# Optimization experiments

Measured on AMD Instinct MI355X. Metric: run time of the kernel, lower is better.

The kernel has to match this reference:

```python
import jax, jax.numpy as jnp
import numpy as np
from jax import lax

# ---- static problem constants (match init_kwargs / call_args) ----
T0 = 0.0
T1 = 5_184_000.0            # 60 days in seconds
DT = 60.0                   # Euler step (s)
DT_FORCING = 3600.0         # hourly wind forcing (s)
DTK = 518_400.0             # 6-day reduced-basis window (s)
NSUB = int(DT_FORCING // DT)             # 60 substeps per forcing step
NFORCING = int((T1 - T0) // DT_FORCING)  # 1440 forcing steps
NDT = len(np.arange(T0, T1, DTK))        # 10 basis knots
NL = 1                                   # layers -> K has NL*2 components


def setup_inputs() -> dict:
    key = jax.random.key(0)
    k1, k2, k3 = jax.random.split(key, 3)
    # K = exp(pk); mean -8 keeps exp(pk)*DT << 1 (stable explicit Euler)
    pk = jax.random.normal(k1, (NDT * NL * 2,), jnp.float32) * 0.5 - 8.0
    TAx = jax.random.normal(k2, (NFORCING,), jnp.float32) * 0.1  # wind stress x
    TAy = jax.random.normal(k3, (NFORCING,), jnp.float32) * 0.1  # wind stress y
    fc = jnp.float32(1e-4)  # Coriolis frequency (s^-1)
    return {"pk": pk, "TAx": TAx, "TAy": TAy, "fc": fc}


def _basis_matrix(dtype):
    # pkt2Kt_matrix with base='gauss'
    gptime = jnp.arange(T0 + DTK / 2, T1 + DTK / 2, DTK)   # (NDT,)
    gtime = jnp.arange(T0, T1, DT_FORCING)                 # (NFORCING,)
    distt = gtime[:, None] - gptime[None, :]               # (NFORCING, NDT)
    tmp = jnp.exp(-0.5 * distt ** 2 / DTK ** 2)
    M = tmp / jnp.sum(tmp, axis=1, keepdims=True)
    return M.astype(dtype)


def _forward(pk, TAx, TAy, fc):
    K = jnp.exp(pk).reshape(NDT, NL * 2)          # kt_1D_to_2D
    Kt = _basis_matrix(pk.dtype) @ K               # (NFORCING, NL*2)
    n = TAx.shape[0]

    def vector_field(t, U, V):
        it = (t // DT).astype(jnp.int32)
        itf = it // NSUB
        aa = jnp.mod(it, NSUB) / NSUB
        itsup = jnp.where(itf + 1 >= n, -1, itf + 1)
        tax = (1 - aa) * TAx[itf] + aa * TAx[itsup]
        tay = (1 - aa) * TAy[itf] + aa * TAy[itsup]
        # NB: Kt[it-1] with it up to NFORCING*NSUB relies on jax clamping
        # out-of-range gathers to the last row, exactly as the original.
        Ktnow = (1 - aa) * Kt[it - 1] + aa * Kt[itsup]
        d_U = fc * V + Ktnow[0] * tax - Ktnow[1] * U
        d_V = -fc * U + Ktnow[0] * tay - Ktnow[1] * V
        return d_U, d_V

    def inner(carry, iin):
        U, V, iout = carry
        t = iout * DT_FORCING + iin * DT
        d_U, d_V = vector_field(t, U, V)
        return (U + DT * d_U, V + DT * d_V, iout), None

    def outer(carry, iout):
        U, V = carry
        (u, v, _), _ = lax.scan(inner, (U[iout], V[iout], iout),
                                jnp.arange(NSUB))
        # final update at index NFORCING is out of bounds -> dropped by jax,
        # matching the original module's semantics
        U = U.at[iout + 1].set(u)
        V = V.at[iout + 1].set(v)
        return (U, V), None

    U0 = jnp.zeros(NFORCING, pk.dtype)
    V0 = jnp.zeros(NFORCING, pk.dtype)
    (U, V), _ = lax.scan(outer, (U0, V0), jnp.arange(NFORCING))
    return U, V


def reference(pk, TAx, TAy, fc):
    return _forward(pk, TAx, TAy, fc)
```

## Files before the change

kernel.cpp:

```cpp
#include <hip/hip_runtime.h>
#include <math.h>

#define NF    1440
#define NWIN  1439
#define NSUB  60
#define NDTK  10
#define BLK   256
#define NBLK  6
#define NWAVE (BLK / 64)
#define B0WIN 216
#define TOKEN 0x5AB1A5CAu


__device__ __forceinline__ float2 kt_row(int i, const float* __restrict__ K0,
                                         const float* __restrict__ K1) {
    const float CEXP = -0.5f / 268738560000.0f;
    float gt = 3600.0f * (float)i;
    float s = 0.0f, a0 = 0.0f, a1 = 0.0f;
    #pragma unroll
    for (int j = 0; j < NDTK; ++j) {
        float d = gt - (259200.0f + 518400.0f * (float)j);
        float e = __expf((d * d) * CEXP);
        s += e;
        a0 = fmaf(e, K0[j], a0);
        a1 = fmaf(e, K1[j], a1);
    }
    return make_float2(a0 / s, a1 / s);
}

__device__ __forceinline__ float4 fast_window(float2 ktl, float2 ks,
    float taxa, float dtax, float taya, float dtay, float ci)
{
    const float DT = 60.0f, H = 1.0f / 60.0f;
    const float dk0 = ks.x - ktl.x, dk1 = ks.y - ktl.y;
    const float g0  = DT * ktl.x,  g1  = DT * dk0;
    float cr  = fmaf(-DT, ktl.y, 1.0f);
    const float crinc = (-DT * dk1) * H;
    const float qr1 = fmaf(g0, dtax, g1 * taxa);
    const float qr2 = g1 * dtax;
    const float qi1 = fmaf(g0, dtay, g1 * taya);
    const float qi2 = g1 * dtay;
    float dr  = g0 * taxa;
    float di  = g0 * taya;
    float drD = fmaf(qr2, H * H, qr1 * H);
    float diD = fmaf(qi2, H * H, qi1 * H);
    const float drD2 = 2.0f * qr2 * H * H;
    const float diD2 = 2.0f * qi2 * H * H;
    float Ar = 1.0f, Ai = 0.0f, Br = 0.0f, Bi = 0.0f;
    #pragma unroll 4
    for (int iin = 0; iin < NSUB; ++iin) {
        const float t1 = ci * Ai;
        const float nAr = fmaf(cr, Ar, -t1);
        const float t2 = ci * Ar;
        const float nAi = fmaf(cr, Ai, t2);
        const float t3 = fmaf(-ci, Bi, dr);
        const float nBr = fmaf(cr, Br, t3);
        const float t4 = fmaf(ci, Br, di);
        const float nBi = fmaf(cr, Bi, t4);
        Ar = nAr; Ai = nAi; Br = nBr; Bi = nBi;
        cr += crinc;
        dr += drD; drD += drD2;
        di += diD; diD += diD2;
    }
    return make_float4(Ar, Ai, Br, Bi);
}

__global__ __launch_bounds__(BLK) void slab_lookback_kernel(
    const float* __restrict__ pk,
    const float* __restrict__ TAx,
    const float* __restrict__ TAy,
    const float* __restrict__ fcp,
    float4* __restrict__ agg,
    unsigned int* __restrict__ flags,
    float* __restrict__ out)
{
    const int t    = threadIdx.x;
    const int b    = blockIdx.x;
    const int lane = t & 63;
    const int wid  = t >> 6;
    const float DT = 60.0f;
    const float fc = fcp[0];
    const float ci = -DT * fc;
    const float H  = 1.0f / 60.0f;

    __shared__ float2 sKt[NF];
    __shared__ float4 wagg[NWAVE];
    __shared__ float4 sagg[NBLK];

    float K0[NDTK], K1[NDTK];
    #pragma unroll
    for (int j = 0; j < NDTK; ++j) {
        K0[j] = __expf(pk[2 * j]);
        K1[j] = __expf(pk[2 * j + 1]);
    }

    float Ar = 1.0f, Ai = 0.0f, Br = 0.0f, Bi = 0.0f;
    int ow = -1;

    if (b == 0) {
        for (int i = t; i < NF; i += BLK) sKt[i] = kt_row(i, K0, K1);
        __syncthreads();

        if (t < 64) {
            if (t < 48) {
                const int w = t >> 1;
                const int h = t & 1;
                const float2 ks  = sKt[w + 1];
                const float taxa = TAx[w], dtax = TAx[w + 1] - taxa;
                const float taya = TAy[w], dtay = TAy[w + 1] - taya;
                float fi = (float)(h * 30);
                int   it = w * NSUB + h * 30;
                #pragma unroll 4
                for (int i = 0; i < 30; ++i, ++it) {
                    const int row = (it == 0) ? (NF - 1) : (it - 1);
                    const float2 kta = sKt[row];
                    const float aa  = fi * H;
                    fi += 1.0f;
                    const float tax = fmaf(aa, dtax, taxa);
                    const float tay = fmaf(aa, dtay, taya);
                    const float kt0 = fmaf(aa, ks.x - kta.x, kta.x);
                    const float kt1 = fmaf(aa, ks.y - kta.y, kta.y);
                    const float cr  = fmaf(-DT, kt1, 1.0f);
                    const float g   = DT * kt0;
                    const float dr  = g * tax;
                    const float di  = g * tay;
                    const float t1 = ci * Ai;
                    const float nAr = fmaf(cr, Ar, -t1);
                    const float t2 = ci * Ar;
                    const float nAi = fmaf(cr, Ai, t2);
                    const float t3 = fmaf(-ci, Bi, dr);
                    const float nBr = fmaf(cr, Br, t3);
                    const float t4 = fmaf(ci, Br, di);
                    const float nBi = fmaf(cr, Bi, t4);
                    Ar = nAr; Ai = nAi; Br = nBr; Bi = nBi;
                }
            }
            const float oAr = __shfl_xor(Ar, 1), oAi = __shfl_xor(Ai, 1);
            const float oBr = __shfl_xor(Br, 1), oBi = __shfl_xor(Bi, 1);
            const float cAr = oAr * Ar - oAi * Ai;
            const float cAi = oAr * Ai + oAi * Ar;
            const float cBr = fmaf(oAr, Br, fmaf(-oAi, Bi, oBr));
            const float cBi = fmaf(oAr, Bi, fmaf(oAi, Br, oBi));
            const int src = (2 * t) & 63;
            Ar = __shfl(cAr, src); Ai = __shfl(cAi, src);
            Br = __shfl(cBr, src); Bi = __shfl(cBi, src);
            if (t < 24) {
                ow = t;
            } else {
                Ar = 1.0f; Ai = 0.0f; Br = 0.0f; Bi = 0.0f;
            }
        } else {
            const int w = t - 40;
            const float2 ktl = sKt[NF - 1];
            const float2 ks  = sKt[w + 1];
            const float taxa = TAx[w], dtax = TAx[w + 1] - taxa;
            const float taya = TAy[w], dtay = TAy[w + 1] - taya;
            const float4 W = fast_window(ktl, ks, taxa, dtax, taya, dtay, ci);
            Ar = W.x; Ai = W.y; Br = W.z; Bi = W.w;
            ow = w;
        }
    } else {
        const int w = B0WIN + (b - 1) * BLK + t;
        if (w < NWIN) {
            const float2 ktl = kt_row(NF - 1, K0, K1);
            const float2 ks  = kt_row(w + 1, K0, K1);
            const float taxa = TAx[w], dtax = TAx[w + 1] - taxa;
            const float taya = TAy[w], dtay = TAy[w + 1] - taya;
            const float4 W = fast_window(ktl, ks, taxa, dtax, taya, dtay, ci);
            Ar = W.x; Ai = W.y; Br = W.z; Bi = W.w;
            ow = w;
        }
    }

    float sAr = Ar, sAi = Ai, sBr = Br, sBi = Bi;
    #pragma unroll
    for (int d = 1; d < 64; d <<= 1) {
        const float oAr = __shfl_up(sAr, d);
        const float oAi = __shfl_up(sAi, d);
        const float oBr = __shfl_up(sBr, d);
        const float oBi = __shfl_up(sBi, d);
        if (lane >= d) {
            const float nAr = sAr * oAr - sAi * oAi;
            const float nAi = sAr * oAi + sAi * oAr;
            const float nBr = fmaf(sAr, oBr, fmaf(-sAi, oBi, sBr));
            const float nBi = fmaf(sAr, oBi, fmaf(sAi, oBr, sBi));
            sAr = nAr; sAi = nAi; sBr = nBr; sBi = nBi;
        }
    }
    if (lane == 63) wagg[wid] = make_float4(sAr, sAi, sBr, sBi);
    __syncthreads();

    float eAr = 1.0f, eAi = 0.0f, eBr = 0.0f, eBi = 0.0f;
    for (int q = 0; q < wid; ++q) {
        const float4 g = wagg[q];
        const float nAr = g.x * eAr - g.y * eAi;
        const float nAi = g.x * eAi + g.y * eAr;
        const float nBr = g.x * eBr - g.y * eBi + g.z;
        const float nBi = g.x * eBi + g.y * eBr + g.w;
        eAr = nAr; eAi = nAi; eBr = nBr; eBi = nBi;
    }
    const float tAr = sAr * eAr - sAi * eAi;
    const float tAi = sAr * eAi + sAi * eAr;
    const float tBr = fmaf(sAr, eBr, fmaf(-sAi, eBi, sBr));
    const float tBi = fmaf(sAr, eBi, fmaf(sAi, eBr, sBi));

    if (t == BLK - 1) {
        agg[b] = make_float4(tAr, tAi, tBr, tBi);
        __threadfence();
        __hip_atomic_store(&flags[b], TOKEN, __ATOMIC_RELEASE,
                           __HIP_MEMORY_SCOPE_AGENT);
    }

    if (t < b) {
        while (__hip_atomic_load(&flags[t], __ATOMIC_ACQUIRE,
                                 __HIP_MEMORY_SCOPE_AGENT) != TOKEN) {
            __builtin_amdgcn_s_sleep(1);
        }
        sagg[t] = agg[t];
    }
    __syncthreads();

    float zr = 0.0f, zi = 0.0f;
    for (int j = 0; j < b; ++j) {
        const float4 g = sagg[j];
        const float nzr = fmaf(g.x, zr, fmaf(-g.y, zi, g.z));
        const float nzi = fmaf(g.x, zi, fmaf(g.y, zr, g.w));
        zr = nzr; zi = nzi;
    }

    if (ow >= 0) {
        const float ozr = fmaf(tAr, zr, fmaf(-tAi, zi, tBr));
        const float ozi = fmaf(tAr, zi, fmaf(tAi, zr, tBi));
        out[ow + 1]      = ozr;
        out[NF + ow + 1] = ozi;
    }
    if (b == 0 && t == 0) {
        out[0]  = 0.0f;
        out[NF] = 0.0f;
    }
}

extern "C" void kernel_launch(void* const* d_in, const int* in_sizes, int n_in,
                              void* d_out, int out_size, void* d_ws, size_t ws_size,
                              hipStream_t stream) {
    const float* pk  = (const float*)d_in[0];
    const float* TAx = (const float*)d_in[1];
    const float* TAy = (const float*)d_in[2];
    const float* fcp = (const float*)d_in[3];
    float* out = (float*)d_out;

    float4* agg = (float4*)d_ws;
    unsigned int* flags = (unsigned int*)((char*)d_ws + NBLK * 16);

    slab_lookback_kernel<<<NBLK, BLK, 0, stream>>>(pk, TAx, TAy, fcp,
                                                   agg, flags, out);
}
```

Baseline: 11.30 us.

## Split each window's 60 substeps across two lanes and double block count

Each forcing window's 60-step affine recurrence is now split into two 30-step halves computed by adjacent lanes, combined with a shuffle-xor compose, and the grid grows from 6 to 12 blocks. This halves the serial per-thread chain length, which dominates latency in this small kernel. In exchange, more blocks take part in the decoupled lookback (a longer serial chain of flag waits and aggregate composition), and half the lanes sit idle during the scan. The interpolation start offset for the second half is folded into the initial cr/dr/di terms.

```diff
diff --git a/kernel.cpp b/kernel.cpp
--- a/kernel.cpp
+++ b/kernel.cpp
@@ -6,9 +6,9 @@
 #define NSUB  60
 #define NDTK  10
 #define BLK   256
-#define NBLK  6
+#define NBLK  12
 #define NWAVE (BLK / 64)
-#define B0WIN 216
+#define B0WIN 120
 #define TOKEN 0x5AB1A5CAu
 
 
@@ -28,27 +28,29 @@
     return make_float2(a0 / s, a1 / s);
 }
 
-__device__ __forceinline__ float4 fast_window(float2 ktl, float2 ks,
-    float taxa, float dtax, float taya, float dtay, float ci)
+__device__ __forceinline__ float4 fast_half(float2 ktl, float2 ks,
+    float taxa, float dtax, float taya, float dtay, float ci, float aa0)
 {
     const float DT = 60.0f, H = 1.0f / 60.0f;
     const float dk0 = ks.x - ktl.x, dk1 = ks.y - ktl.y;
     const float g0  = DT * ktl.x,  g1  = DT * dk0;
-    float cr  = fmaf(-DT, ktl.y, 1.0f);
-    const float crinc = (-DT * dk1) * H;
+    const float cr1 = -DT * dk1;
+    float cr  = fmaf(cr1, aa0, fmaf(-DT, ktl.y, 1.0f));
+    const float crinc = cr1 * H;
     const float qr1 = fmaf(g0, dtax, g1 * taxa);
     const float qr2 = g1 * dtax;
     const float qi1 = fmaf(g0, dtay, g1 * taya);
     const float qi2 = g1 * dtay;
-    float dr  = g0 * taxa;
-    float di  = g0 * taya;
-    float drD = fmaf(qr2, H * H, qr1 * H);
-    float diD = fmaf(qi2, H * H, qi1 * H);
+    float dr  = fmaf(fmaf(qr2, aa0, qr1), aa0, g0 * taxa);
+    float di  = fmaf(fmaf(qi2, aa0, qi1), aa0, g0 * taya);
+    const float dstep = (2.0f * aa0 + H) * H;
+    float drD = fmaf(qr2, dstep, qr1 * H);
+    float diD = fmaf(qi2, dstep, qi1 * H);
     const float drD2 = 2.0f * qr2 * H * H;
     const float diD2 = 2.0f * qi2 * H * H;
     float Ar = 1.0f, Ai = 0.0f, Br = 0.0f, Bi = 0.0f;
-    #pragma unroll 4
-    for (int iin = 0; iin < NSUB; ++iin) {
+    #pragma unroll 5
+    for (int iin = 0; iin < 30; ++iin) {
         const float t1 = ci * Ai;
         const float nAr = fmaf(cr, Ar, -t1);
         const float t2 = ci * Ar;
@@ -95,80 +97,82 @@
     }
 
     float Ar = 1.0f, Ai = 0.0f, Br = 0.0f, Bi = 0.0f;
-    int ow = -1;
+    int myw = -1;
 
     if (b == 0) {
         for (int i = t; i < NF; i += BLK) sKt[i] = kt_row(i, K0, K1);
         __syncthreads();
 
-        if (t < 64) {
-            if (t < 48) {
-                const int w = t >> 1;
-                const int h = t & 1;
-                const float2 ks  = sKt[w + 1];
-                const float taxa = TAx[w], dtax = TAx[w + 1] - taxa;
-                const float taya = TAy[w], dtay = TAy[w + 1] - taya;
-                float fi = (float)(h * 30);
-                int   it = w * NSUB + h * 30;
-                #pragma unroll 4
-                for (int i = 0; i < 30; ++i, ++it) {
-                    const int row = (it == 0) ? (NF - 1) : (it - 1);
-                    const float2 kta = sKt[row];
-                    const float aa  = fi * H;
-                    fi += 1.0f;
-                    const float tax = fmaf(aa, dtax, taxa);
-                    const float tay = fmaf(aa, dtay, taya);
-                    const float kt0 = fmaf(aa, ks.x - kta.x, kta.x);
-                    const float kt1 = fmaf(aa, ks.y - kta.y, kta.y);
-                    const float cr  = fmaf(-DT, kt1, 1.0f);
-                    const float g   = DT * kt0;
-                    const float dr  = g * tax;
-                    const float di  = g * tay;
-                    const float t1 = ci * Ai;
-                    const float nAr = fmaf(cr, Ar, -t1);
-                    const float t2 = ci * Ar;
-                    const float nAi = fmaf(cr, Ai, t2);
-                    const float t3 = fmaf(-ci, Bi, dr);
-                    const float nBr = fmaf(cr, Br, t3);
-                    const float t4 = fmaf(ci, Br, di);
-                    const float nBi = fmaf(cr, Bi, t4);
-                    Ar = nAr; Ai = nAi; Br = nBr; Bi = nBi;
-                }
+        if (t < 48) {
+            const int w = t >> 1;
+            const int h = t & 1;
+            const float2 ks  = sKt[w + 1];
+            const float taxa = TAx[w], dtax = TAx[w + 1] - taxa;
+            const float taya = TAy[w], dtay = TAy[w + 1] - taya;
+            float fi = (float)(h * 30);
+            int   it = w * NSUB + h * 30;
+            #pragma unroll 5
+            for (int i = 0; i < 30; ++i, ++it) {
+                const int row = (it == 0) ? (NF - 1) : (it - 1);
+                const float2 kta = sKt[row];
+                const float aa  = fi * H;
+                fi += 1.0f;
+                const float tax = fmaf(aa, dtax, taxa);
+                const float tay = fmaf(aa, dtay, taya);
+                const float kt0 = fmaf(aa, ks.x - kta.x, kta.x);
+                const float kt1 = fmaf(aa, ks.y - kta.y, kta.y);
+                const float cr  = fmaf(-DT, kt1, 1.0f);
+                const float g   = DT * kt0;
+                const float dr  = g * tax;
+                const float di  = g * tay;
+                const float t1 = ci * Ai;
+                const float nAr = fmaf(cr, Ar, -t1);
+                const float t2 = ci * Ar;
+                const float nAi = fmaf(cr, Ai, t2);
+                const float t3 = fmaf(-ci, Bi, dr);
+                const float nBr = fmaf(cr, Br, t3);
+                const float t4 = fmaf(ci, Br, di);
+                const float nBi = fmaf(cr, Bi, t4);
+                Ar = nAr; Ai = nAi; Br = nBr; Bi = nBi;
             }
-            const float oAr = __shfl_xor(Ar, 1), oAi = __shfl_xor(Ai, 1);
-            const float oBr = __shfl_xor(Br, 1), oBi = __shfl_xor(Bi, 1);
-            const float cAr = oAr * Ar - oAi * Ai;
-            const float cAi = oAr * Ai + oAi * Ar;
-            const float cBr = fmaf(oAr, Br, fmaf(-oAi, Bi, oBr));
-            const float cBi = fmaf(oAr, Bi, fmaf(oAi, Br, oBi));
-            const int src = (2 * t) & 63;
-            Ar = __shfl(cAr, src); Ai = __shfl(cAi, src);
-            Br = __shfl(cBr, src); Bi = __shfl(cBi, src);
-            if (t < 24) {
-                ow = t;
-            } else {
-                Ar = 1.0f; Ai = 0.0f; Br = 0.0f; Bi = 0.0f;
-            }
-        } else {
-            const int w = t - 40;
+            myw = w;
+        } else if (t >= 64) {
+            const int w = 24 + ((t - 64) >> 1);
             const float2 ktl = sKt[NF - 1];
             const float2 ks  = sKt[w + 1];
             const float taxa = TAx[w], dtax = TAx[w + 1] - taxa;
             const float taya = TAy[w], dtay = TAy[w + 1] - taya;
-            const float4 W = fast_window(ktl, ks, taxa, dtax, taya, dtay, ci);
+            const float4 W = fast_half(ktl, ks, taxa, dtax, taya, dtay, ci,
+                                       0.5f * (float)(t & 1));
             Ar = W.x; Ai = W.y; Br = W.z; Bi = W.w;
-            ow = w;
+            myw = w;
         }
     } else {
-        const int w = B0WIN + (b - 1) * BLK + t;
+        const int w = B0WIN + (b - 1) * 128 + (t >> 1);
         if (w < NWIN) {
             const float2 ktl = kt_row(NF - 1, K0, K1);
             const float2 ks  = kt_row(w + 1, K0, K1);
             const float taxa = TAx[w], dtax = TAx[w + 1] - taxa;
             const float taya = TAy[w], dtay = TAy[w + 1] - taya;
-            const float4 W = fast_window(ktl, ks, taxa, dtax, taya, dtay, ci);
+            const float4 W = fast_half(ktl, ks, taxa, dtax, taya, dtay, ci,
+                                       0.5f * (float)(t & 1));
             Ar = W.x; Ai = W.y; Br = W.z; Bi = W.w;
-            ow = w;
+            myw = w;
+        }
+    }
+
+    {
+        const float oAr = __shfl_xor(Ar, 1), oAi = __shfl_xor(Ai, 1);
+        const float oBr = __shfl_xor(Br, 1), oBi = __shfl_xor(Bi, 1);
+        const float cAr = oAr * Ar - oAi * Ai;
+        const float cAi = oAr * Ai + oAi * Ar;
+        const float cBr = fmaf(oAr, Br, fmaf(-oAi, Bi, oBr));
+        const float cBi = fmaf(oAr, Bi, fmaf(oAi, Br, oBi));
+        if (((t & 1) == 0) && myw >= 0) {
+            Ar = cAr; Ai = cAi; Br = cBr; Bi = cBi;
+        } else {
+            Ar = 1.0f; Ai = 0.0f; Br = 0.0f; Bi = 0.0f;
+            myw = -1;
         }
     }
 
@@ -228,11 +232,11 @@
         zr = nzr; zi = nzi;
     }
 
-    if (ow >= 0) {
+    if (myw >= 0) {
         const float ozr = fmaf(tAr, zr, fmaf(-tAi, zi, tBr));
         const float ozi = fmaf(tAr, zi, fmaf(tAi, zr, tBi));
-        out[ow + 1]      = ozr;
-        out[NF + ow + 1] = ozi;
+        out[myw + 1]      = ozr;
+        out[NF + myw + 1] = ozi;
     }
     if (b == 0 && t == 0) {
         out[0]  = 0.0f;
```

New measurement: 10.54 us. 1.07x faster.
